# Performance work log

Measured on AMD Instinct MI355X. Metric: run time of the kernel, lower is better.

## Reference

```python
import jax, jax.numpy as jnp
import numpy as np

LAMBDA_L1, LAMBDA_IOU, LAMBDA_CLS = 5.0, 2.0, 1.0
B, N, K, M = 16, 900, 91, 100


def setup_inputs() -> dict:
    key = jax.random.key(0)
    k1, k2, k3, k4, k5, k6 = jax.random.split(key, 6)
    cls_pred = jax.random.normal(k1, (B, N, K), dtype=jnp.float32)
    # valid xyxy boxes in [0,1]
    pmin = jax.random.uniform(k2, (B, N, 2), dtype=jnp.float32) * 0.5
    pwh = jax.random.uniform(k3, (B, N, 2), dtype=jnp.float32) * 0.5 + 1e-3
    bb_pred = jnp.concatenate([pmin, pmin + pwh], axis=-1)
    gmin = jax.random.uniform(k4, (B, M, 2), dtype=jnp.float32) * 0.5
    gwh = jax.random.uniform(k5, (B, M, 2), dtype=jnp.float32) * 0.5 + 1e-3
    bb_gt = jnp.concatenate([gmin, gmin + gwh], axis=-1)
    cls_gt = jax.random.randint(k6, (B, M), 0, K)
    return {"cls_pred": cls_pred, "bb_pred": bb_pred, "cls_gt": cls_gt, "bb_gt": bb_gt}


def _box_iou(b1, b2):
    # b1 [P,4], b2 [Q,4] -> iou [P,Q]
    area1 = (b1[:, 2] - b1[:, 0]) * (b1[:, 3] - b1[:, 1])
    area2 = (b2[:, 2] - b2[:, 0]) * (b2[:, 3] - b2[:, 1])
    x_min = jnp.maximum(b1[:, None, 0], b2[None, :, 0])
    y_min = jnp.maximum(b1[:, None, 1], b2[None, :, 1])
    x_max = jnp.minimum(b1[:, None, 2], b2[None, :, 2])
    y_max = jnp.minimum(b1[:, None, 3], b2[None, :, 3])
    inter = jnp.clip(x_max - x_min, 0) * jnp.clip(y_max - y_min, 0)
    union = area1[:, None] + area2[None, :] - inter
    return inter / (union + 1e-6)


def _solve(cost):
    # Jonker-Volgenant shortest augmenting path; cost (n, m) with n <= m; minimization.
    n, m = cost.shape
    u = np.zeros(n + 1)
    v = np.zeros(m + 1)
    p = np.zeros(m + 1, dtype=np.int64)   # p[j] = row matched to col j (1-indexed)
    way = np.zeros(m + 1, dtype=np.int64)
    for i in range(1, n + 1):
        p[0] = i
        j0 = 0
        minv = np.full(m + 1, np.inf)
        used = np.zeros(m + 1, dtype=bool)
        while True:
            used[j0] = True
            i0 = p[j0]
            cur = cost[i0 - 1] - u[i0] - v[1:]
            cur = np.where(used[1:], np.inf, cur)
            upd = cur < minv[1:]
            minv[1:] = np.where(upd, cur, minv[1:])
            way[1:] = np.where(upd, j0, way[1:])
            cand = np.where(used[1:], np.inf, minv[1:])
            j1 = int(np.argmin(cand)) + 1
            delta = cand[j1 - 1]
            uj = np.nonzero(used)[0]
            u[p[uj]] += delta
            v[uj] -= delta
            minv[1:] = np.where(used[1:], minv[1:], minv[1:] - delta)
            j0 = j1
            if p[j0] == 0:
                break
        while j0 != 0:
            j1 = way[j0]
            p[j0] = p[j1]
            j0 = j1
    cols = np.nonzero(p[1:])[0]
    rows = p[1:][cols] - 1
    return rows, cols


def _linear_sum_assignment(cost):
    cost = np.asarray(cost, dtype=np.float64)
    transposed = cost.shape[0] > cost.shape[1]
    rows, cols = _solve(cost.T if transposed else cost)
    if transposed:
        rows, cols = cols, rows
    order = np.argsort(rows)
    return rows[order], cols[order]


def reference(cls_pred, bb_pred, cls_gt, bb_gt):
    b, n, k = cls_pred.shape
    m = cls_gt.shape[1]
    out_prob = jax.nn.softmax(cls_pred.reshape(b * n, k), axis=-1)
    out_bbox = bb_pred.reshape(b * n, 4)
    tgt_ids = cls_gt.reshape(-1)
    tgt_bbox = bb_gt.reshape(-1, 4)
    cost_class = -out_prob[:, tgt_ids]                                   # [B*N, B*M]
    l1 = jnp.sum(jnp.abs(out_bbox[:, None, :] - tgt_bbox[None, :, :]), -1)  # p=1 cdist
    iou = -_box_iou(out_bbox, tgt_bbox)
    C = LAMBDA_IOU * iou + LAMBDA_L1 * l1 + LAMBDA_CLS * cost_class
    C = np.asarray(C.reshape(b, n, b, m))
    Cb = C[np.arange(b), :, np.arange(b), :]  # diagonal blocks [B, N, M] (= torch split(sizes)[i][i])
    preds, tgts = [], []
    for bi in range(b):
        r, c = _linear_sum_assignment(Cb[bi])
        preds.append(r)
        tgts.append(c)
    return (jnp.asarray(np.stack(preds), dtype=jnp.int64),
            jnp.asarray(np.stack(tgts), dtype=jnp.int64))
```

## Files before the change

kernel.cpp:

```cpp
#include <hip/hip_runtime.h>
#include <math.h>

#define NB 16
#define NP 900
#define NC 91
#define NT 100
#define SLOTS 15

__global__ __launch_bounds__(256) void softmax_stats_kernel(
    const float* __restrict__ cls_pred,
    float2* __restrict__ stats,
    unsigned* __restrict__ colOwner)
{
    const int gtid = blockIdx.x * 256 + threadIdx.x;
    if (gtid < NB * NP) colOwner[gtid] = 0xFFFFFFFFu;

    const int wave = gtid >> 6;
    const int lane = threadIdx.x & 63;
    if (wave >= NB * NP) return;
    const float* crow = cls_pred + (size_t)wave * NC;

    const float x0 = crow[lane];
    const float x1 = (lane + 64 < NC) ? crow[lane + 64] : -INFINITY;
    float mx = fmaxf(x0, x1);
    #pragma unroll
    for (int off = 32; off >= 1; off >>= 1)
        mx = fmaxf(mx, __shfl_xor(mx, off, 64));

    float s = expf(x0 - mx);
    if (lane + 64 < NC) s += expf(x1 - mx);
    #pragma unroll
    for (int off = 32; off >= 1; off >>= 1)
        s += __shfl_xor(s, off, 64);

    if (lane == 0) stats[wave] = make_float2(mx, 1.0f / s);
}

__global__ __launch_bounds__(256) void costrow_kernel(
    const float* __restrict__ cls_pred,
    const float* __restrict__ bb_pred,
    const int*   __restrict__ cls_gt,
    const float* __restrict__ bb_gt,
    const float2* __restrict__ stats,
    float* __restrict__ Ct,
    float* __restrict__ u_init,
    int*   __restrict__ amin,
    unsigned* __restrict__ colOwner)
{
    const int row  = (blockIdx.x * 256 + threadIdx.x) >> 6;
    const int lane = threadIdx.x & 63;
    if (row >= NB * NT) return;
    const int b = row / NT;

    const float4 gt = *reinterpret_cast<const float4*>(bb_gt + (size_t)row*4);
    const float garea = (gt.z - gt.x) * (gt.w - gt.y);
    const int   c     = cls_gt[row];

    float* outr = Ct + (size_t)row * NP;
    float best = INFINITY; int bj = 0;

    #pragma unroll
    for (int r = 0; r < SLOTS; ++r) {
        const int n = 64*r + lane;
        if ((r < SLOTS-1) || (lane < 4)) {
            const float4 bp = *reinterpret_cast<const float4*>(bb_pred + ((size_t)b*NP + n)*4);
            const float2 st = stats[b*NP + n];
            const float  x  = cls_pred[((size_t)(b*NP + n))*NC + c];

            const float l1 = fabsf(bp.x - gt.x) + fabsf(bp.y - gt.y) +
                             fabsf(bp.z - gt.z) + fabsf(bp.w - gt.w);
            const float parea = (bp.z - bp.x) * (bp.w - bp.y);
            const float xm = fmaxf(bp.x, gt.x);
            const float ym = fmaxf(bp.y, gt.y);
            const float xM = fminf(bp.z, gt.z);
            const float yM = fminf(bp.w, gt.w);
            const float inter = fmaxf(xM - xm, 0.f) * fmaxf(yM - ym, 0.f);
            const float iou = inter / (parea + garea - inter + 1e-6f);
            const float pc  = expf(x - st.x) * st.y;

            const float cost = 5.0f*l1 - 2.0f*iou - pc;
            outr[n] = cost;
            if (cost < best) { best = cost; bj = n; }
        }
    }

    float vmin = best;
    #pragma unroll
    for (int off = 32; off >= 1; off >>= 1)
        vmin = fminf(vmin, __shfl_xor(vmin, off, 64));
    const unsigned long long win = __ballot(best == vmin);
    const int bjAll = __shfl(bj, __builtin_ctzll(win), 64);
    if (lane == 0) {
        u_init[row] = vmin;
        amin[row]   = bjAll;
        atomicMin(&colOwner[(size_t)b*NP + bjAll], (unsigned)(row % NT));
    }
}

__device__ __forceinline__ int pop_row(unsigned long long& fm0, unsigned long long& fm1)
{
    if (fm0) { const int l = __builtin_ctzll(fm0); fm0 &= fm0 - 1; return l + 1;  }
    if (fm1) { const int l = __builtin_ctzll(fm1); fm1 &= fm1 - 1; return l + 65; }
    return 0;
}

__global__ __launch_bounds__(64) void jv_kernel(
    const float* __restrict__ Ct,
    const float* __restrict__ u_init,
    const int*   __restrict__ amin,
    const unsigned* __restrict__ colOwner,
    int* __restrict__ out)
{
    const int b    = blockIdx.x;
    const int lane = threadIdx.x;
    const float* Cb = Ct + (size_t)b*NT*NP;

    double v[SLOTS], minv[SLOTS];
    float  cw[SLOTS], cnext[SLOTS];
    int    way[SLOTS], p[SLOTS];

    double u0 = (double)u_init[b*NT + lane];
    double u1 = (lane < NT-64) ? (double)u_init[b*NT + 64 + lane] : 0.0;

    #pragma unroll
    for (int r = 0; r < SLOTS; ++r) {
        v[r] = 0.0; way[r] = 0;
        unsigned o = 0xFFFFFFFFu;
        if ((r < SLOTS-1) || (lane < 4)) o = colOwner[(size_t)b*NP + 64*r + lane];
        p[r] = (o == 0xFFFFFFFFu) ? 0 : (int)o + 1;
    }

    const int a0 = amin[b*NT + lane];
    const bool as0 = (colOwner[(size_t)b*NP + a0] == (unsigned)lane);
    bool as1 = true;
    if (lane < NT-64) {
        const int a1 = amin[b*NT + 64 + lane];
        as1 = (colOwner[(size_t)b*NP + a1] == (unsigned)(64 + lane));
    }
    unsigned long long fm0 = __ballot(!as0);
    unsigned long long fm1 = __ballot(!as1 && (lane < NT-64));

    int iCur = pop_row(fm0, fm1);
    if (iCur) {
        const float* cr = Cb + (size_t)(iCur-1)*NP;
        #pragma unroll
        for (int r = 0; r < SLOTS; ++r) {
            int ja = 64*r + lane; if (ja > NP-1) ja = NP-1;
            cnext[r] = cr[ja];
        }
    }

    while (iCur) {
        const int iNext = pop_row(fm0, fm1);

        unsigned usedMask = 0;
        bool it0 = false, it1 = false;
        double Dtot = 0.0;
        #pragma unroll
        for (int r = 0; r < SLOTS; ++r) { minv[r] = INFINITY; cw[r] = cnext[r]; }

        const int i = iCur;
        if (i <= 64) { if (lane == i-1)  it0 = true; }
        else         { if (lane == i-65) it1 = true; }
        double ui0 = (i <= 64) ? __shfl(u0, i-1, 64) : __shfl(u1, i-65, 64);

        if (iNext) {
            const float* cr = Cb + (size_t)(iNext-1)*NP;
            #pragma unroll
            for (int r = 0; r < SLOTS; ++r) {
                int ja = 64*r + lane; if (ja > NP-1) ja = NP-1;
                cnext[r] = cr[ja];
            }
        }

        int j0 = 0, jfinal;
        while (true) {
            double best = INFINITY;
            int    pk   = 0;
            #pragma unroll
            for (int r = 0; r < SLOTS; ++r) {
                const int jm1 = 64*r + lane;
                const bool valid = ((r < SLOTS-1) || (lane < 4)) && !((usedMask >> r) & 1u);
                const double cur = valid ? (((double)cw[r] - ui0) - v[r]) : INFINITY;
                if (cur < minv[r]) { minv[r] = cur; way[r] = j0; }
                if (minv[r] < best) { best = minv[r]; pk = (jm1 + 1) | (p[r] << 10); }
            }
            double vmin = best;
            #pragma unroll
            for (int off = 32; off >= 1; off >>= 1)
                vmin = fmin(vmin, __shfl_xor(vmin, off, 64));
            const unsigned long long win = __ballot(best == vmin);
            pk = __shfl(pk, __builtin_ctzll(win), 64);

            const double delta = vmin;
            const int    j1    = pk & 1023;
            const int    pnext = pk >> 10;
            Dtot += delta;
            #pragma unroll
            for (int r = 0; r < SLOTS; ++r) minv[r] -= delta;

            #pragma unroll
            for (int r = 0; r < SLOTS; ++r) {
                if (64*r + lane + 1 == j1) {
                    usedMask |= 1u << r;
                    minv[r] = INFINITY;
                    v[r] += Dtot;
                }
            }

            if (pnext == 0) { jfinal = j1; break; }

            ui0 = (pnext <= 64) ? __shfl(u0, pnext-1, 64) : __shfl(u1, pnext-65, 64);
            if (pnext <= 64) { if (lane == pnext-1)  { u0 -= Dtot; it0 = true; } }
            else             { if (lane == pnext-65) { u1 -= Dtot; it1 = true; } }

            {
                const float* cr = Cb + (size_t)(pnext-1)*NP;
                #pragma unroll
                for (int r = 0; r < SLOTS; ++r) {
                    int ja = 64*r + lane; if (ja > NP-1) ja = NP-1;
                    cw[r] = cr[ja];
                }
            }
            j0 = j1;
        }

        {
            int jc = jfinal;
            while (jc != 0) {
                int wsel = 0;
                #pragma unroll
                for (int r = 0; r < SLOTS; ++r)
                    if (64*r + lane + 1 == jc) wsel = way[r];
                const int jprev = __shfl(wsel, (jc-1) & 63, 64);
                int newrow;
                if (jprev == 0) newrow = i;
                else {
                    int psel = 0;
                    #pragma unroll
                    for (int r = 0; r < SLOTS; ++r)
                        if (64*r + lane + 1 == jprev) psel = p[r];
                    newrow = __shfl(psel, (jprev-1) & 63, 64);
                }
                #pragma unroll
                for (int r = 0; r < SLOTS; ++r)
                    if (64*r + lane + 1 == jc) p[r] = newrow;
                jc = jprev;
            }
        }

        #pragma unroll
        for (int r = 0; r < SLOTS; ++r)
            if ((usedMask >> r) & 1u) v[r] -= Dtot;
        if (it0) u0 += Dtot;
        if (it1) u1 += Dtot;

        iCur = iNext;
    }

    int base = 0;
    #pragma unroll
    for (int r = 0; r < SLOTS; ++r) {
        const unsigned long long mask = __ballot(p[r] != 0);
        if (p[r] != 0) {
            const int rank = base + (int)__popcll(mask & ((1ull << lane) - 1ull));
            out[b*NT + rank]         = 64*r + lane;
            out[NB*NT + b*NT + rank] = p[r] - 1;
        }
        base += (int)__popcll(mask);
    }
}

extern "C" void kernel_launch(void* const* d_in, const int* in_sizes, int n_in,
                              void* d_out, int out_size, void* d_ws, size_t ws_size,
                              hipStream_t stream)
{
    const float* cls_pred = (const float*)d_in[0];
    const float* bb_pred  = (const float*)d_in[1];
    const int*   cls_gt   = (const int*)d_in[2];
    const float* bb_gt    = (const float*)d_in[3];

    char* base = (char*)d_ws;
    const size_t ctBytes    = (size_t)NB*NT*NP*sizeof(float);
    const size_t statsBytes = (size_t)NB*NP*sizeof(float2);
    float*    Ct       = (float*)base;
    float2*   stats    = (float2*)(base + ctBytes);
    unsigned* colOwner = (unsigned*)(base + ctBytes + statsBytes);
    float*    u_init   = (float*)(base + ctBytes + statsBytes + (size_t)NB*NP*4);
    int*      aminP    = (int*)(base + ctBytes + statsBytes + (size_t)NB*NP*4 + (size_t)NB*NT*4);

    softmax_stats_kernel<<<(NB*NP + 3)/4, 256, 0, stream>>>(cls_pred, stats, colOwner);
    costrow_kernel<<<(NB*NT + 3)/4, 256, 0, stream>>>(
        cls_pred, bb_pred, cls_gt, bb_gt, stats, Ct, u_init, aminP, colOwner);
    jv_kernel<<<NB, 64, 0, stream>>>(Ct, u_init, aminP, colOwner, (int*)d_out);
}
```

Baseline: 54.99 us.

## Fuse softmax stats, cost matrix, and JV solver into one per-batch kernel

Merges the three launches into a single kernel with one 512-thread block per batch. Softmax stats, column owners and initial duals now live in shared memory instead of global workspace, which removes two launch gaps and the global round trips. The cost is parallelism: the softmax and cost-row phases now run on only 16 blocks. Softmax uses one thread per row with serial 91-element loops, replacing the former one-wave-per-row reduction, so this phase may be much slower.

```diff
diff --git a/kernel.cpp b/kernel.cpp
--- a/kernel.cpp
+++ b/kernel.cpp
@@ -7,140 +7,118 @@
 #define NT 100
 #define SLOTS 15
 
-__global__ __launch_bounds__(256) void softmax_stats_kernel(
-    const float* __restrict__ cls_pred,
-    float2* __restrict__ stats,
-    unsigned* __restrict__ colOwner)
-{
-    const int gtid = blockIdx.x * 256 + threadIdx.x;
-    if (gtid < NB * NP) colOwner[gtid] = 0xFFFFFFFFu;
-
-    const int wave = gtid >> 6;
-    const int lane = threadIdx.x & 63;
-    if (wave >= NB * NP) return;
-    const float* crow = cls_pred + (size_t)wave * NC;
-
-    const float x0 = crow[lane];
-    const float x1 = (lane + 64 < NC) ? crow[lane + 64] : -INFINITY;
-    float mx = fmaxf(x0, x1);
-    #pragma unroll
-    for (int off = 32; off >= 1; off >>= 1)
-        mx = fmaxf(mx, __shfl_xor(mx, off, 64));
-
-    float s = expf(x0 - mx);
-    if (lane + 64 < NC) s += expf(x1 - mx);
-    #pragma unroll
-    for (int off = 32; off >= 1; off >>= 1)
-        s += __shfl_xor(s, off, 64);
-
-    if (lane == 0) stats[wave] = make_float2(mx, 1.0f / s);
-}
-
-__global__ __launch_bounds__(256) void costrow_kernel(
+__global__ __launch_bounds__(512) void hungarian_fused_kernel(
     const float* __restrict__ cls_pred,
     const float* __restrict__ bb_pred,
     const int*   __restrict__ cls_gt,
     const float* __restrict__ bb_gt,
-    const float2* __restrict__ stats,
     float* __restrict__ Ct,
-    float* __restrict__ u_init,
-    int*   __restrict__ amin,
-    unsigned* __restrict__ colOwner)
-{
-    const int row  = (blockIdx.x * 256 + threadIdx.x) >> 6;
-    const int lane = threadIdx.x & 63;
-    if (row >= NB * NT) return;
-    const int b = row / NT;
-
-    const float4 gt = *reinterpret_cast<const float4*>(bb_gt + (size_t)row*4);
-    const float garea = (gt.z - gt.x) * (gt.w - gt.y);
-    const int   c     = cls_gt[row];
-
-    float* outr = Ct + (size_t)row * NP;
-    float best = INFINITY; int bj = 0;
-
-    #pragma unroll
-    for (int r = 0; r < SLOTS; ++r) {
-        const int n = 64*r + lane;
-        if ((r < SLOTS-1) || (lane < 4)) {
-            const float4 bp = *reinterpret_cast<const float4*>(bb_pred + ((size_t)b*NP + n)*4);
-            const float2 st = stats[b*NP + n];
-            const float  x  = cls_pred[((size_t)(b*NP + n))*NC + c];
-
-            const float l1 = fabsf(bp.x - gt.x) + fabsf(bp.y - gt.y) +
-                             fabsf(bp.z - gt.z) + fabsf(bp.w - gt.w);
-            const float parea = (bp.z - bp.x) * (bp.w - bp.y);
-            const float xm = fmaxf(bp.x, gt.x);
-            const float ym = fmaxf(bp.y, gt.y);
-            const float xM = fminf(bp.z, gt.z);
-            const float yM = fminf(bp.w, gt.w);
-            const float inter = fmaxf(xM - xm, 0.f) * fmaxf(yM - ym, 0.f);
-            const float iou = inter / (parea + garea - inter + 1e-6f);
-            const float pc  = expf(x - st.x) * st.y;
-
-            const float cost = 5.0f*l1 - 2.0f*iou - pc;
-            outr[n] = cost;
-            if (cost < best) { best = cost; bj = n; }
-        }
-    }
-
-    float vmin = best;
-    #pragma unroll
-    for (int off = 32; off >= 1; off >>= 1)
-        vmin = fminf(vmin, __shfl_xor(vmin, off, 64));
-    const unsigned long long win = __ballot(best == vmin);
-    const int bjAll = __shfl(bj, __builtin_ctzll(win), 64);
-    if (lane == 0) {
-        u_init[row] = vmin;
-        amin[row]   = bjAll;
-        atomicMin(&colOwner[(size_t)b*NP + bjAll], (unsigned)(row % NT));
-    }
-}
-
-__device__ __forceinline__ int pop_row(unsigned long long& fm0, unsigned long long& fm1)
-{
-    if (fm0) { const int l = __builtin_ctzll(fm0); fm0 &= fm0 - 1; return l + 1;  }
-    if (fm1) { const int l = __builtin_ctzll(fm1); fm1 &= fm1 - 1; return l + 65; }
-    return 0;
-}
-
-__global__ __launch_bounds__(64) void jv_kernel(
-    const float* __restrict__ Ct,
-    const float* __restrict__ u_init,
-    const int*   __restrict__ amin,
-    const unsigned* __restrict__ colOwner,
     int* __restrict__ out)
 {
     const int b    = blockIdx.x;
-    const int lane = threadIdx.x;
+    const int tid  = threadIdx.x;
+    const int wid  = tid >> 6;
+    const int lane = tid & 63;
+
+    __shared__ float2   sstats[NP];
+    __shared__ unsigned sOwner[NP];
+    __shared__ float    sU[NT];
+    __shared__ int      sAmin[NT];
+
+    for (int j = tid; j < NP; j += 512) sOwner[j] = 0xFFFFFFFFu;
+
+    const float* cpb = cls_pred + (size_t)b*NP*NC;
+    for (int n = tid; n < NP; n += 512) {
+        const float* crow = cpb + (size_t)n*NC;
+        float mx = -INFINITY;
+        for (int k = 0; k < NC; ++k) mx = fmaxf(mx, crow[k]);
+        float s = 0.f;
+        for (int k = 0; k < NC; ++k) s += expf(crow[k] - mx);
+        sstats[n] = make_float2(mx, 1.0f / s);
+    }
+    __syncthreads();
+
+    for (int m = wid; m < NT; m += 8) {
+        const int row = b*NT + m;
+        const float4 gt = *reinterpret_cast<const float4*>(bb_gt + (size_t)row*4);
+        const float garea = (gt.z - gt.x) * (gt.w - gt.y);
+        const int   c     = cls_gt[row];
+
+        float* outr = Ct + (size_t)row * NP;
+        float best = INFINITY; int bj = 0;
+
+        #pragma unroll
+        for (int r = 0; r < SLOTS; ++r) {
+            const int n = 64*r + lane;
+            if ((r < SLOTS-1) || (lane < 4)) {
+                const float4 bp = *reinterpret_cast<const float4*>(bb_pred + ((size_t)b*NP + n)*4);
+                const float2 st = sstats[n];
+                const float  x  = cpb[(size_t)n*NC + c];
+
+                const float l1 = fabsf(bp.x - gt.x) + fabsf(bp.y - gt.y) +
+                                 fabsf(bp.z - gt.z) + fabsf(bp.w - gt.w);
+                const float parea = (bp.z - bp.x) * (bp.w - bp.y);
+                const float xm = fmaxf(bp.x, gt.x);
+                const float ym = fmaxf(bp.y, gt.y);
+                const float xM = fminf(bp.z, gt.z);
+                const float yM = fminf(bp.w, gt.w);
+                const float inter = fmaxf(xM - xm, 0.f) * fmaxf(yM - ym, 0.f);
+                const float iou = inter / (parea + garea - inter + 1e-6f);
+                const float pc  = expf(x - st.x) * st.y;
+
+                const float cost = 5.0f*l1 - 2.0f*iou - pc;
+                outr[n] = cost;
+                if (cost < best) { best = cost; bj = n; }
+            }
+        }
+
+        float vmin = best;
+        #pragma unroll
+        for (int off = 32; off >= 1; off >>= 1)
+            vmin = fminf(vmin, __shfl_xor(vmin, off, 64));
+        const unsigned long long win = __ballot(best == vmin);
+        const int bjAll = __shfl(bj, __builtin_ctzll(win), 64);
+        if (lane == 0) {
+            sU[m]    = vmin;
+            sAmin[m] = bjAll;
+            atomicMin(&sOwner[bjAll], (unsigned)m);
+        }
+    }
+    __syncthreads();
+
+    if (wid != 0) return;
+
     const float* Cb = Ct + (size_t)b*NT*NP;
 
     double v[SLOTS], minv[SLOTS];
     float  cw[SLOTS], cnext[SLOTS];
     int    way[SLOTS], p[SLOTS];
 
-    double u0 = (double)u_init[b*NT + lane];
-    double u1 = (lane < NT-64) ? (double)u_init[b*NT + 64 + lane] : 0.0;
+    double u0 = (double)sU[lane];
+    double u1 = (lane < NT-64) ? (double)sU[64 + lane] : 0.0;
 
     #pragma unroll
     for (int r = 0; r < SLOTS; ++r) {
         v[r] = 0.0; way[r] = 0;
         unsigned o = 0xFFFFFFFFu;
-        if ((r < SLOTS-1) || (lane < 4)) o = colOwner[(size_t)b*NP + 64*r + lane];
+        if ((r < SLOTS-1) || (lane < 4)) o = sOwner[64*r + lane];
         p[r] = (o == 0xFFFFFFFFu) ? 0 : (int)o + 1;
     }
 
-    const int a0 = amin[b*NT + lane];
-    const bool as0 = (colOwner[(size_t)b*NP + a0] == (unsigned)lane);
+    const int a0 = sAmin[lane];
+    const bool as0 = (sOwner[a0] == (unsigned)lane);
     bool as1 = true;
     if (lane < NT-64) {
-        const int a1 = amin[b*NT + 64 + lane];
-        as1 = (colOwner[(size_t)b*NP + a1] == (unsigned)(64 + lane));
+        const int a1 = sAmin[64 + lane];
+        as1 = (sOwner[a1] == (unsigned)(64 + lane));
     }
     unsigned long long fm0 = __ballot(!as0);
     unsigned long long fm1 = __ballot(!as1 && (lane < NT-64));
 
-    int iCur = pop_row(fm0, fm1);
+    int iCur = 0;
+    if (fm0)      { const int l = __builtin_ctzll(fm0); fm0 &= fm0-1; iCur = l + 1;  }
+    else if (fm1) { const int l = __builtin_ctzll(fm1); fm1 &= fm1-1; iCur = l + 65; }
+
     if (iCur) {
         const float* cr = Cb + (size_t)(iCur-1)*NP;
         #pragma unroll
@@ -151,7 +129,9 @@
     }
 
     while (iCur) {
-        const int iNext = pop_row(fm0, fm1);
+        int iNext = 0;
+        if (fm0)      { const int l = __builtin_ctzll(fm0); fm0 &= fm0-1; iNext = l + 1;  }
+        else if (fm1) { const int l = __builtin_ctzll(fm1); fm1 &= fm1-1; iNext = l + 65; }
 
         unsigned usedMask = 0;
         bool it0 = false, it1 = false;
@@ -280,17 +260,8 @@
     const int*   cls_gt   = (const int*)d_in[2];
     const float* bb_gt    = (const float*)d_in[3];
 
-    char* base = (char*)d_ws;
-    const size_t ctBytes    = (size_t)NB*NT*NP*sizeof(float);
-    const size_t statsBytes = (size_t)NB*NP*sizeof(float2);
-    float*    Ct       = (float*)base;
-    float2*   stats    = (float2*)(base + ctBytes);
-    unsigned* colOwner = (unsigned*)(base + ctBytes + statsBytes);
-    float*    u_init   = (float*)(base + ctBytes + statsBytes + (size_t)NB*NP*4);
-    int*      aminP    = (int*)(base + ctBytes + statsBytes + (size_t)NB*NP*4 + (size_t)NB*NT*4);
-
-    softmax_stats_kernel<<<(NB*NP + 3)/4, 256, 0, stream>>>(cls_pred, stats, colOwner);
-    costrow_kernel<<<(NB*NT + 3)/4, 256, 0, stream>>>(
-        cls_pred, bb_pred, cls_gt, bb_gt, stats, Ct, u_init, aminP, colOwner);
-    jv_kernel<<<NB, 64, 0, stream>>>(Ct, u_init, aminP, colOwner, (int*)d_out);
+    float* Ct = (float*)d_ws;
+
+    hungarian_fused_kernel<<<NB, 512, 0, stream>>>(
+        cls_pred, bb_pred, cls_gt, bb_gt, Ct, (int*)d_out);
 }
```

New measurement: 115.6 us. 2.1x slower.
